# Kernel tuning notes

Hardware: AMD Instinct MI355X
Metric: run time of the kernel (lower is better)

Reference implementation:

```python
import jax, jax.numpy as jnp
import numpy as np

N, D, H = 4_000_000, 10, 16

def setup_inputs() -> dict:
    key = jax.random.key(0)
    k1, k2, k3, k4, k5 = jax.random.split(key, 5)
    x = jax.random.normal(k1, (N, D), dtype=jnp.float32)
    # torch nn.Linear default init: U(-1/sqrt(fan_in), 1/sqrt(fan_in))
    lim1 = 1.0 / np.sqrt(D)
    lim2 = 1.0 / np.sqrt(H)
    W1 = jax.random.uniform(k2, (H, D), dtype=jnp.float32, minval=-lim1, maxval=lim1)
    b1 = jax.random.uniform(k3, (H,), dtype=jnp.float32, minval=-lim1, maxval=lim1)
    W2 = jax.random.uniform(k4, (1, H), dtype=jnp.float32, minval=-lim2, maxval=lim2)
    b2 = jax.random.uniform(k5, (1,), dtype=jnp.float32, minval=-lim2, maxval=lim2)
    return {"x": x, "W1": W1, "b1": b1, "W2": W2, "b2": b2}

def reference(x, W1, b1, W2, b2):
    gram = x.T @ x                      # [10,10] symmetric Gram matrix
    v, w = jnp.linalg.eigh(gram)        # eigenvalues ascending; w: [10,10]
    y = jnp.maximum(w @ W1.T + b1, 0.0) # fc1 + ReLU -> [10,16]
    y = y @ W2.T + b2                   # fc2 -> [10,1]
    return 0.5 * (jax.nn.sigmoid(y) + 1.0)
```

## Files before the change

### kernel.cpp

```cpp
#include <hip/hip_runtime.h>
#include <math.h>


#define BLK2 256
#define GRID2 1024

__global__ void zero_ws_kernel(double* __restrict__ g) {
  int t = threadIdx.x;
  if (t < 55) g[t] = 0.0;
}

__global__ __launch_bounds__(BLK2) void gram_kernel(const float* __restrict__ x,
                                                    double* __restrict__ g,
                                                    int npairs) {
  float acc[55];
#pragma unroll
  for (int k = 0; k < 55; k++) acc[k] = 0.0f;

  int tid = blockIdx.x * BLK2 + threadIdx.x;
  const int stride = GRID2 * BLK2;

  for (int p = tid; p < npairs; p += stride) {
    const float4* base = (const float4*)(x + (size_t)p * 20);
    float4 q0 = base[0], q1 = base[1], q2 = base[2], q3 = base[3], q4 = base[4];
    float v[20] = {q0.x, q0.y, q0.z, q0.w, q1.x, q1.y, q1.z, q1.w,
                   q2.x, q2.y, q2.z, q2.w, q3.x, q3.y, q3.z, q3.w,
                   q4.x, q4.y, q4.z, q4.w};
    int k = 0;
#pragma unroll
    for (int i = 0; i < 10; i++) {
#pragma unroll
      for (int j = 0; j <= i; j++) {
        acc[k] += v[i] * v[j] + v[10 + i] * v[10 + j];
        k++;
      }
    }
  }

  __shared__ double sred[4][55];
  int lane = threadIdx.x & 63;
  int wv = threadIdx.x >> 6;
#pragma unroll
  for (int k = 0; k < 55; k++) {
    double d = (double)acc[k];
#pragma unroll
    for (int off = 32; off > 0; off >>= 1) d += __shfl_down(d, off, 64);
    if (lane == 0) sred[wv][k] = d;
  }
  __syncthreads();
  if (threadIdx.x < 55) {
    double s = sred[0][threadIdx.x] + sred[1][threadIdx.x] +
               sred[2][threadIdx.x] + sred[3][threadIdx.x];
    atomicAdd(&g[threadIdx.x], s);
  }
}


__device__ __forceinline__ float sf_sign(float a, float b) {
  return (b >= 0.0f) ? fabsf(a) : -fabsf(a);
}

__device__ __forceinline__ float slapy2(float x, float y) {
  float xa = fabsf(x), ya = fabsf(y);
  float w = fmaxf(xa, ya), z = fminf(xa, ya);
  if (z == 0.0f) return w;
  float q = z / w;
  return w * sqrtf(1.0f + q * q);
}

__device__ __forceinline__ void slartg(float f, float g, float* c, float* s, float* r) {
  if (g == 0.0f) {
    *c = 1.0f; *s = 0.0f; *r = f;
  } else if (f == 0.0f) {
    *c = 0.0f; *s = sf_sign(1.0f, g); *r = fabsf(g);
  } else {
    float d = sqrtf(f * f + g * g);
    *c = fabsf(f) / d;
    float rr = sf_sign(d, f);
    *s = g / rr;
    *r = rr;
  }
}

__device__ __forceinline__ void slaev2(float a, float b, float c,
                                       float* rt1, float* rt2, float* cs1, float* sn1) {
  float sm = a + c;
  float df = a - c;
  float adf = fabsf(df);
  float tb = b + b;
  float ab = fabsf(tb);
  float acmx, acmn;
  if (fabsf(a) > fabsf(c)) { acmx = a; acmn = c; } else { acmx = c; acmn = a; }
  float rt;
  if (adf > ab)      { float t = ab / adf; rt = adf * sqrtf(1.0f + t * t); }
  else if (adf < ab) { float t = adf / ab; rt = ab * sqrtf(1.0f + t * t); }
  else               { rt = ab * sqrtf(2.0f); }
  int sgn1;
  if (sm < 0.0f) {
    *rt1 = 0.5f * (sm - rt); sgn1 = -1;
    *rt2 = (acmx / *rt1) * acmn - (b / *rt1) * b;
  } else if (sm > 0.0f) {
    *rt1 = 0.5f * (sm + rt); sgn1 = 1;
    *rt2 = (acmx / *rt1) * acmn - (b / *rt1) * b;
  } else {
    *rt1 = 0.5f * rt; *rt2 = -0.5f * rt; sgn1 = 1;
  }
  int sgn2;
  float cs;
  if (df >= 0.0f) { cs = df + rt; sgn2 = 1; } else { cs = df - rt; sgn2 = -1; }
  float acs = fabsf(cs);
  if (acs > ab) {
    float ct = -tb / cs;
    *sn1 = 1.0f / sqrtf(1.0f + ct * ct);
    *cs1 = ct * (*sn1);
  } else {
    if (ab == 0.0f) { *cs1 = 1.0f; *sn1 = 0.0f; }
    else {
      float tn = -cs / tb;
      *cs1 = 1.0f / sqrtf(1.0f + tn * tn);
      *sn1 = tn * (*cs1);
    }
  }
  if (sgn1 == sgn2) { float tn = *cs1; *cs1 = -(*sn1); *sn1 = tn; }
}

__device__ __forceinline__ float sel10(const float* a, int idx0) {
  float v = 0.0f;
#pragma unroll
  for (int k = 0; k < 10; k++) if (k == idx0) v = a[k];
  return v;
}
__device__ __forceinline__ void put10(float* a, int idx0, float v) {
#pragma unroll
  for (int k = 0; k < 10; k++) if (k == idx0) a[k] = v;
}

#define A_(r, c) Am[((r)-1) * 10 + ((c)-1)]
#define Z_(r, c) Zm[((r)-1) * 10 + ((c)-1)]
#define D_(i) dv[(i)-1]
#define E_(i) ev[(i)-1]
#define TAUV(i) tauv[(i)-1]
#define WV(i) wvv[(i)-1]
#define CS_(i) csv[(i)-1]
#define SN_(i) snv[(i)-1]

__global__ __launch_bounds__(64, 1) void eig_mlp_kernel(
    const double* __restrict__ g,
    const float* __restrict__ W1,
    const float* __restrict__ b1,
    const float* __restrict__ W2,
    const float* __restrict__ b2,
    float* __restrict__ out) {
  if (threadIdx.x != 0 || blockIdx.x != 0) return;
  const int n = 10;
  float Am[100], Zm[100];
  float dv[10], ev[10], tauv[10], wvv[10], csv[10], snv[10];

  {
    int k = 0;
#pragma unroll
    for (int i = 0; i < 10; i++)
#pragma unroll
      for (int j = 0; j <= i; j++) {
        float v = (float)g[k++];
        Am[i * 10 + j] = v;
        Am[j * 10 + i] = v;
      }
  }

#pragma unroll
  for (int i = 1; i <= n - 1; i++) {
    const int nmi = n - i;
    float alpha = A_(i + 1, i);
    float taui = 0.0f;
    if (nmi > 1) {
      float ss = 0.0f;
#pragma unroll
      for (int r = i + 2; r <= n; r++) { float t = A_(r, i); ss += t * t; }
      float xnorm = sqrtf(ss);
      if (xnorm != 0.0f) {
        float beta = -sf_sign(slapy2(alpha, xnorm), alpha);
        taui = (beta - alpha) / beta;
        float sc = 1.0f / (alpha - beta);
#pragma unroll
        for (int r = i + 2; r <= n; r++) A_(r, i) *= sc;
        alpha = beta;
      }
    }
    E_(i) = alpha;
    A_(i + 1, i) = alpha;
    if (taui != 0.0f) {
      A_(i + 1, i) = 1.0f;
#pragma unroll
      for (int r = i + 1; r <= n; r++) {
        float s = 0.0f;
#pragma unroll
        for (int c = i + 1; c <= n; c++) {
          float arc = (r >= c) ? A_(r, c) : A_(c, r);
          s += arc * A_(c, i);
        }
        WV(r) = taui * s;
      }
      float dot = 0.0f;
#pragma unroll
      for (int r = i + 1; r <= n; r++) dot += WV(r) * A_(r, i);
      float al2 = -0.5f * taui * dot;
#pragma unroll
      for (int r = i + 1; r <= n; r++) WV(r) += al2 * A_(r, i);
#pragma unroll
      for (int c = i + 1; c <= n; c++)
#pragma unroll
        for (int r = c; r <= n; r++)
          A_(r, c) -= A_(r, i) * WV(c) + WV(r) * A_(c, i);
      A_(i + 1, i) = E_(i);
    }
    D_(i) = A_(i, i);
    TAUV(i) = taui;
  }
  D_(n) = A_(n, n);

#pragma unroll
  for (int r = 1; r <= n; r++)
#pragma unroll
    for (int c = 1; c <= n; c++) Z_(r, c) = (r == c) ? 1.0f : 0.0f;
#pragma unroll
  for (int i = n - 1; i >= 1; i--) {
    float taui = TAUV(i);
    if (taui != 0.0f) {
#pragma unroll
      for (int c = 1; c <= n; c++) {
        float t = Z_(i + 1, c);
#pragma unroll
        for (int r = i + 2; r <= n; r++) t += A_(r, i) * Z_(r, c);
        t *= taui;
        Z_(i + 1, c) -= t;
#pragma unroll
        for (int r = i + 2; r <= n; r++) Z_(r, c) -= A_(r, i) * t;
      }
    }
  }

  const float eps = 5.9604644775390625e-08f;
  const float eps2 = eps * eps;
  const float safmin = 1.17549435082228751e-38f;
  const int nmaxit = n * 30;
  int jtot = 0;
  int l1 = 1;
  int guard = 0;

  while (l1 <= n && guard++ < 2000) {
    int m;
    if (l1 > 1) put10(ev, l1 - 2, 0.0f);
    {
      bool found = false;
      int mf = n;
#pragma unroll
      for (int k = 1; k <= n - 1; k++) {
        if (!found && k >= l1) {
          float tst = fabsf(ev[k - 1]);
          if (tst == 0.0f) {
            mf = k; found = true;
          } else if (tst <= (sqrtf(fabsf(dv[k - 1])) * sqrtf(fabsf(dv[k]))) * eps) {
            ev[k - 1] = 0.0f;
            mf = k; found = true;
          }
        }
      }
      m = found ? mf : n;
    }
    int l = l1, lsv = l, lend = m, lendsv = m;
    l1 = m + 1;
    if (lend == l) continue;
    if (fabsf(sel10(dv, lend - 1)) < fabsf(sel10(dv, l - 1))) { lend = lsv; l = lendsv; }

    if (lend > l) {
      for (;;) {
        if (guard++ > 4000) break;
        int m2;
        if (l != lend) {
          bool found = false;
          int mf = lend;
#pragma unroll
          for (int k = 1; k <= n - 1; k++) {
            if (!found && k >= l && k <= lend - 1) {
              float tst = ev[k - 1] * ev[k - 1];
              if (tst <= (eps2 * fabsf(dv[k - 1])) * fabsf(dv[k]) + safmin) {
                mf = k; found = true;
              }
            }
          }
          m2 = found ? mf : lend;
        } else {
          m2 = lend;
        }
        if (m2 < lend) put10(ev, m2 - 1, 0.0f);
        float p = sel10(dv, l - 1);
        if (m2 == l) {
          put10(dv, l - 1, p);
          l = l + 1;
          if (l <= lend) continue;
          break;
        }
        if (m2 == l + 1) {
          float rt1, rt2, c2, s2;
          slaev2(sel10(dv, l - 1), sel10(ev, l - 1), sel10(dv, l), &rt1, &rt2, &c2, &s2);
#pragma unroll
          for (int j = 1; j <= n - 1; j++) {
            if (j == l) {
#pragma unroll
              for (int r = 0; r < n; r++) {
                float t = Zm[r * 10 + j];
                Zm[r * 10 + j]     = c2 * t - s2 * Zm[r * 10 + j - 1];
                Zm[r * 10 + j - 1] = s2 * t + c2 * Zm[r * 10 + j - 1];
              }
            }
          }
          put10(dv, l - 1, rt1);
          put10(dv, l, rt2);
          put10(ev, l - 1, 0.0f);
          l = l + 2;
          if (l <= lend) continue;
          break;
        }
        if (jtot == nmaxit) break;
        jtot++;
        float El = sel10(ev, l - 1);
        float gg = (sel10(dv, l) - p) / (2.0f * El);
        float rr = slapy2(gg, 1.0f);
        gg = sel10(dv, m2 - 1) - p + (El / (gg + sf_sign(rr, gg)));
        float s = 1.0f, c = 1.0f;
        p = 0.0f;
#pragma unroll
        for (int i = n - 1; i >= 1; i--) {
          if (i <= m2 - 1 && i >= l) {
            float f = s * ev[i - 1];
            float b = c * ev[i - 1];
            slartg(gg, f, &c, &s, &rr);
            if (i != m2 - 1) ev[i] = rr;
            gg = dv[i] - p;
            rr = (dv[i - 1] - gg) * s + 2.0f * c * b;
            p = s * rr;
            dv[i] = gg + p;
            gg = c * rr - b;
            csv[i - 1] = c;
            snv[i - 1] = -s;
          }
        }
#pragma unroll
        for (int j = n - 1; j >= 1; j--) {
          if (j <= m2 - 1 && j >= l) {
            float cj = csv[j - 1], sj = snv[j - 1];
#pragma unroll
            for (int r = 0; r < n; r++) {
              float t = Zm[r * 10 + j];
              Zm[r * 10 + j]     = cj * t - sj * Zm[r * 10 + j - 1];
              Zm[r * 10 + j - 1] = sj * t + cj * Zm[r * 10 + j - 1];
            }
          }
        }
        put10(dv, l - 1, sel10(dv, l - 1) - p);
        put10(ev, l - 1, gg);
      }
    } else {
      for (;;) {
        if (guard++ > 4000) break;
        int m2;
        if (l != lend) {
          bool found = false;
          int mf = lend;
#pragma unroll
          for (int k = n; k >= 2; k--) {
            if (!found && k <= l && k >= lend + 1) {
              float tst = ev[k - 2] * ev[k - 2];
              if (tst <= (eps2 * fabsf(dv[k - 1])) * fabsf(dv[k - 2]) + safmin) {
                mf = k; found = true;
              }
            }
          }
          m2 = found ? mf : lend;
        } else {
          m2 = lend;
        }
        if (m2 > lend) put10(ev, m2 - 2, 0.0f);
        float p = sel10(dv, l - 1);
        if (m2 == l) {
          put10(dv, l - 1, p);
          l = l - 1;
          if (l >= lend) continue;
          break;
        }
        if (m2 == l - 1) {
          float rt1, rt2, c2, s2;
          slaev2(sel10(dv, l - 2), sel10(ev, l - 2), sel10(dv, l - 1), &rt1, &rt2, &c2, &s2);
#pragma unroll
          for (int j = 1; j <= n - 1; j++) {
            if (j == l - 1) {
#pragma unroll
              for (int r = 0; r < n; r++) {
                float t = Zm[r * 10 + j];
                Zm[r * 10 + j]     = c2 * t - s2 * Zm[r * 10 + j - 1];
                Zm[r * 10 + j - 1] = s2 * t + c2 * Zm[r * 10 + j - 1];
              }
            }
          }
          put10(dv, l - 2, rt1);
          put10(dv, l - 1, rt2);
          put10(ev, l - 2, 0.0f);
          l = l - 2;
          if (l >= lend) continue;
          break;
        }
        if (jtot == nmaxit) break;
        jtot++;
        float El1 = sel10(ev, l - 2);
        float gg = (sel10(dv, l - 2) - p) / (2.0f * El1);
        float rr = slapy2(gg, 1.0f);
        gg = sel10(dv, m2 - 1) - p + (El1 / (gg + sf_sign(rr, gg)));
        float s = 1.0f, c = 1.0f;
        p = 0.0f;
#pragma unroll
        for (int i = 1; i <= n - 1; i++) {
          if (i >= m2 && i <= l - 1) {
            float f = s * ev[i - 1];
            float b = c * ev[i - 1];
            slartg(gg, f, &c, &s, &rr);
            if (i >= 2) {
              if (i != m2) ev[i - 2] = rr;
            }
            gg = dv[i - 1] - p;
            rr = (dv[i] - gg) * s + 2.0f * c * b;
            p = s * rr;
            dv[i - 1] = gg + p;
            gg = c * rr - b;
            csv[i - 1] = c;
            snv[i - 1] = s;
          }
        }
#pragma unroll
        for (int j = 1; j <= n - 1; j++) {
          if (j >= m2 && j <= l - 1) {
            float cj = csv[j - 1], sj = snv[j - 1];
#pragma unroll
            for (int r = 0; r < n; r++) {
              float t = Zm[r * 10 + j];
              Zm[r * 10 + j]     = cj * t - sj * Zm[r * 10 + j - 1];
              Zm[r * 10 + j - 1] = sj * t + cj * Zm[r * 10 + j - 1];
            }
          }
        }
        put10(dv, l - 1, sel10(dv, l - 1) - p);
        put10(ev, l - 2, gg);
      }
    }
  }

#pragma unroll
  for (int ii = 2; ii <= n; ii++) {
    const int i = ii - 1;
    int k = i;
    float p = dv[i - 1];
#pragma unroll
    for (int j = ii; j <= n; j++) {
      if (dv[j - 1] < p) { k = j; p = dv[j - 1]; }
    }
    if (k != i) {
      float Di = dv[i - 1];
      put10(dv, k - 1, Di);
      dv[i - 1] = p;
#pragma unroll
      for (int kk = 1; kk <= n; kk++) {
        if (kk == k) {
#pragma unroll
          for (int r = 0; r < n; r++) {
            float t = Zm[r * 10 + (i - 1)];
            Zm[r * 10 + (i - 1)] = Zm[r * 10 + (kk - 1)];
            Zm[r * 10 + (kk - 1)] = t;
          }
        }
      }
    }
  }

#pragma unroll
  for (int r = 0; r < 10; r++) {
    double o = (double)b2[0];
#pragma unroll
    for (int h = 0; h < 16; h++) {
      double sgm = (double)b1[h];
#pragma unroll
      for (int k = 0; k < 10; k++) sgm += (double)Zm[r * 10 + k] * (double)W1[h * 10 + k];
      if (sgm > 0.0) o += sgm * (double)W2[h];
    }
    double sig = 1.0 / (1.0 + exp(-o));
    out[r] = (float)(0.5 * (sig + 1.0));
  }
}

extern "C" void kernel_launch(void* const* d_in, const int* in_sizes, int n_in,
                              void* d_out, int out_size, void* d_ws, size_t ws_size,
                              hipStream_t stream) {
  const float* x  = (const float*)d_in[0];
  const float* W1 = (const float*)d_in[1];
  const float* b1 = (const float*)d_in[2];
  const float* W2 = (const float*)d_in[3];
  const float* b2 = (const float*)d_in[4];
  double* g = (double*)d_ws;
  float* out = (float*)d_out;

  int nrows = in_sizes[0] / 10;
  int npairs = nrows / 2;

  zero_ws_kernel<<<1, 64, 0, stream>>>(g);
  gram_kernel<<<GRID2, BLK2, 0, stream>>>(x, g, npairs);
  eig_mlp_kernel<<<1, 64, 0, stream>>>(g, W1, b1, W2, b2, out);
}
```

Measured before the change: 378.0 us.

## Stage Gram loads through LDS, spread atomics, parallelize eigenvector rotations across lanes

The Gram kernel now reads x as fully coalesced float4 tiles into shared memory and then has each thread pick up its own pair of rows, instead of each thread doing strided 80-byte loads. Block results are spread over four atomic target copies to reduce contention, and the eigensolver kernel summs them. The eigensolver now has each of ten lanes own one row of Z, applying Givens rotations to that row only, with runtime-bounded loops instead of fully unrolled masked loops. This adds two extra barriers per tile and dynamic register indexing via select chains.

```diff
diff --git a/kernel.cpp b/kernel.cpp
--- a/kernel.cpp
+++ b/kernel.cpp
@@ -4,25 +4,52 @@
 
 #define BLK2 256
 #define GRID2 1024
+#define TILE_F4 (BLK2 * 5)
 
 __global__ void zero_ws_kernel(double* __restrict__ g) {
   int t = threadIdx.x;
-  if (t < 55) g[t] = 0.0;
-}
-
-__global__ __launch_bounds__(BLK2) void gram_kernel(const float* __restrict__ x,
+  if (t < 220) g[t] = 0.0;
+}
+
+__global__ __launch_bounds__(BLK2) void gram_kernel(const float4* __restrict__ x4,
                                                     double* __restrict__ g,
-                                                    int npairs) {
+                                                    int nf4) {
+  __shared__ float4 tile[TILE_F4];
   float acc[55];
 #pragma unroll
   for (int k = 0; k < 55; k++) acc[k] = 0.0f;
 
-  int tid = blockIdx.x * BLK2 + threadIdx.x;
-  const int stride = GRID2 * BLK2;
-
-  for (int p = tid; p < npairs; p += stride) {
-    const float4* base = (const float4*)(x + (size_t)p * 20);
-    float4 q0 = base[0], q1 = base[1], q2 = base[2], q3 = base[3], q4 = base[4];
+  const int tid = threadIdx.x;
+  const int ntiles = (nf4 + TILE_F4 - 1) / TILE_F4;
+
+  for (int t = blockIdx.x; t < ntiles; t += GRID2) {
+    const int base = t * TILE_F4;
+    float4 r0, r1, r2, r3, r4;
+    {
+      int i0 = base + 0 * BLK2 + tid;
+      int i1 = base + 1 * BLK2 + tid;
+      int i2 = base + 2 * BLK2 + tid;
+      int i3 = base + 3 * BLK2 + tid;
+      int i4 = base + 4 * BLK2 + tid;
+      float4 zz = make_float4(0.f, 0.f, 0.f, 0.f);
+      r0 = (i0 < nf4) ? x4[i0] : zz;
+      r1 = (i1 < nf4) ? x4[i1] : zz;
+      r2 = (i2 < nf4) ? x4[i2] : zz;
+      r3 = (i3 < nf4) ? x4[i3] : zz;
+      r4 = (i4 < nf4) ? x4[i4] : zz;
+    }
+    __syncthreads();
+    tile[0 * BLK2 + tid] = r0;
+    tile[1 * BLK2 + tid] = r1;
+    tile[2 * BLK2 + tid] = r2;
+    tile[3 * BLK2 + tid] = r3;
+    tile[4 * BLK2 + tid] = r4;
+    __syncthreads();
+    float4 q0 = tile[tid * 5 + 0];
+    float4 q1 = tile[tid * 5 + 1];
+    float4 q2 = tile[tid * 5 + 2];
+    float4 q3 = tile[tid * 5 + 3];
+    float4 q4 = tile[tid * 5 + 4];
     float v[20] = {q0.x, q0.y, q0.z, q0.w, q1.x, q1.y, q1.z, q1.w,
                    q2.x, q2.y, q2.z, q2.w, q3.x, q3.y, q3.z, q3.w,
                    q4.x, q4.y, q4.z, q4.w};
@@ -48,10 +75,11 @@
     if (lane == 0) sred[wv][k] = d;
   }
   __syncthreads();
+  double* gr = g + 55 * (blockIdx.x & 3);
   if (threadIdx.x < 55) {
     double s = sred[0][threadIdx.x] + sred[1][threadIdx.x] +
                sred[2][threadIdx.x] + sred[3][threadIdx.x];
-    atomicAdd(&g[threadIdx.x], s);
+    atomicAdd(&gr[threadIdx.x], s);
   }
 }
 
@@ -127,12 +155,12 @@
 __device__ __forceinline__ float sel10(const float* a, int idx0) {
   float v = 0.0f;
 #pragma unroll
-  for (int k = 0; k < 10; k++) if (k == idx0) v = a[k];
+  for (int k = 0; k < 10; k++) v = (k == idx0) ? a[k] : v;
   return v;
 }
 __device__ __forceinline__ void put10(float* a, int idx0, float v) {
 #pragma unroll
-  for (int k = 0; k < 10; k++) if (k == idx0) a[k] = v;
+  for (int k = 0; k < 10; k++) a[k] = (k == idx0) ? v : a[k];
 }
 
 #define A_(r, c) Am[((r)-1) * 10 + ((c)-1)]
@@ -141,8 +169,6 @@
 #define E_(i) ev[(i)-1]
 #define TAUV(i) tauv[(i)-1]
 #define WV(i) wvv[(i)-1]
-#define CS_(i) csv[(i)-1]
-#define SN_(i) snv[(i)-1]
 
 __global__ __launch_bounds__(64, 1) void eig_mlp_kernel(
     const double* __restrict__ g,
@@ -151,7 +177,8 @@
     const float* __restrict__ W2,
     const float* __restrict__ b2,
     float* __restrict__ out) {
-  if (threadIdx.x != 0 || blockIdx.x != 0) return;
+  if (blockIdx.x != 0) return;
+  const int lane = threadIdx.x;
   const int n = 10;
   float Am[100], Zm[100];
   float dv[10], ev[10], tauv[10], wvv[10], csv[10], snv[10];
@@ -162,9 +189,11 @@
     for (int i = 0; i < 10; i++)
 #pragma unroll
       for (int j = 0; j <= i; j++) {
-        float v = (float)g[k++];
-        Am[i * 10 + j] = v;
-        Am[j * 10 + i] = v;
+        double v = g[k] + g[55 + k] + g[110 + k] + g[165 + k];
+        float f = (float)v;
+        Am[i * 10 + j] = f;
+        Am[j * 10 + i] = f;
+        k++;
       }
   }
 
@@ -238,6 +267,16 @@
         for (int r = i + 2; r <= n; r++) Z_(r, c) -= A_(r, i) * t;
       }
     }
+  }
+
+  const int r_own = (lane < 10) ? lane : 0;
+  float z[10];
+#pragma unroll
+  for (int k = 0; k < 10; k++) {
+    float v = Zm[0 * 10 + k];
+#pragma unroll
+    for (int rr = 1; rr < 10; rr++) v = (r_own == rr) ? Zm[rr * 10 + k] : v;
+    z[k] = v;
   }
 
   const float eps = 5.9604644775390625e-08f;
@@ -249,24 +288,16 @@
   int guard = 0;
 
   while (l1 <= n && guard++ < 2000) {
-    int m;
     if (l1 > 1) put10(ev, l1 - 2, 0.0f);
-    {
-      bool found = false;
-      int mf = n;
-#pragma unroll
-      for (int k = 1; k <= n - 1; k++) {
-        if (!found && k >= l1) {
-          float tst = fabsf(ev[k - 1]);
-          if (tst == 0.0f) {
-            mf = k; found = true;
-          } else if (tst <= (sqrtf(fabsf(dv[k - 1])) * sqrtf(fabsf(dv[k]))) * eps) {
-            ev[k - 1] = 0.0f;
-            mf = k; found = true;
-          }
-        }
-      }
-      m = found ? mf : n;
+    int m = n;
+    for (int mm = l1; mm <= n - 1; mm++) {
+      float tst = fabsf(sel10(ev, mm - 1));
+      if (tst == 0.0f) { m = mm; break; }
+      if (tst <= (sqrtf(fabsf(sel10(dv, mm - 1))) * sqrtf(fabsf(sel10(dv, mm)))) * eps) {
+        put10(ev, mm - 1, 0.0f);
+        m = mm;
+        break;
+      }
     }
     int l = l1, lsv = l, lend = m, lendsv = m;
     l1 = m + 1;
@@ -276,22 +307,15 @@
     if (lend > l) {
       for (;;) {
         if (guard++ > 4000) break;
-        int m2;
+        int m2 = lend;
         if (l != lend) {
-          bool found = false;
-          int mf = lend;
-#pragma unroll
-          for (int k = 1; k <= n - 1; k++) {
-            if (!found && k >= l && k <= lend - 1) {
-              float tst = ev[k - 1] * ev[k - 1];
-              if (tst <= (eps2 * fabsf(dv[k - 1])) * fabsf(dv[k]) + safmin) {
-                mf = k; found = true;
-              }
+          for (int mm = l; mm <= lend - 1; mm++) {
+            float e = sel10(ev, mm - 1);
+            if (e * e <= (eps2 * fabsf(sel10(dv, mm - 1))) * fabsf(sel10(dv, mm)) + safmin) {
+              m2 = mm;
+              break;
             }
           }
-          m2 = found ? mf : lend;
-        } else {
-          m2 = lend;
         }
         if (m2 < lend) put10(ev, m2 - 1, 0.0f);
         float p = sel10(dv, l - 1);
@@ -304,17 +328,10 @@
         if (m2 == l + 1) {
           float rt1, rt2, c2, s2;
           slaev2(sel10(dv, l - 1), sel10(ev, l - 1), sel10(dv, l), &rt1, &rt2, &c2, &s2);
-#pragma unroll
-          for (int j = 1; j <= n - 1; j++) {
-            if (j == l) {
-#pragma unroll
-              for (int r = 0; r < n; r++) {
-                float t = Zm[r * 10 + j];
-                Zm[r * 10 + j]     = c2 * t - s2 * Zm[r * 10 + j - 1];
-                Zm[r * 10 + j - 1] = s2 * t + c2 * Zm[r * 10 + j - 1];
-              }
-            }
-          }
+          float a = sel10(z, l);
+          float b = sel10(z, l - 1);
+          put10(z, l, c2 * a - s2 * b);
+          put10(z, l - 1, s2 * a + c2 * b);
           put10(dv, l - 1, rt1);
           put10(dv, l, rt2);
           put10(ev, l - 1, 0.0f);
@@ -330,33 +347,28 @@
         gg = sel10(dv, m2 - 1) - p + (El / (gg + sf_sign(rr, gg)));
         float s = 1.0f, c = 1.0f;
         p = 0.0f;
-#pragma unroll
-        for (int i = n - 1; i >= 1; i--) {
-          if (i <= m2 - 1 && i >= l) {
-            float f = s * ev[i - 1];
-            float b = c * ev[i - 1];
-            slartg(gg, f, &c, &s, &rr);
-            if (i != m2 - 1) ev[i] = rr;
-            gg = dv[i] - p;
-            rr = (dv[i - 1] - gg) * s + 2.0f * c * b;
-            p = s * rr;
-            dv[i] = gg + p;
-            gg = c * rr - b;
-            csv[i - 1] = c;
-            snv[i - 1] = -s;
+        for (int i = m2 - 1; i >= l; i--) {
+          float e = sel10(ev, i - 1);
+          float f = s * e, b = c * e;
+          slartg(gg, f, &c, &s, &rr);
+          if (i != m2 - 1) put10(ev, i, rr);
+          gg = sel10(dv, i) - p;
+          rr = (sel10(dv, i - 1) - gg) * s + 2.0f * c * b;
+          p = s * rr;
+          put10(dv, i, gg + p);
+          gg = c * rr - b;
+          put10(csv, i - 1, c);
+          put10(snv, i - 1, -s);
+        }
+        {
+          float a = sel10(z, m2 - 1);
+          for (int j = m2 - 1; j >= l; j--) {
+            float cj = sel10(csv, j - 1), sj = sel10(snv, j - 1);
+            float b = sel10(z, j - 1);
+            put10(z, j, cj * a - sj * b);
+            a = sj * a + cj * b;
           }
-        }
-#pragma unroll
-        for (int j = n - 1; j >= 1; j--) {
-          if (j <= m2 - 1 && j >= l) {
-            float cj = csv[j - 1], sj = snv[j - 1];
-#pragma unroll
-            for (int r = 0; r < n; r++) {
-              float t = Zm[r * 10 + j];
-              Zm[r * 10 + j]     = cj * t - sj * Zm[r * 10 + j - 1];
-              Zm[r * 10 + j - 1] = sj * t + cj * Zm[r * 10 + j - 1];
-            }
-          }
+          put10(z, l - 1, a);
         }
         put10(dv, l - 1, sel10(dv, l - 1) - p);
         put10(ev, l - 1, gg);
@@ -364,22 +376,15 @@
     } else {
       for (;;) {
         if (guard++ > 4000) break;
-        int m2;
+        int m2 = lend;
         if (l != lend) {
-          bool found = false;
-          int mf = lend;
-#pragma unroll
-          for (int k = n; k >= 2; k--) {
-            if (!found && k <= l && k >= lend + 1) {
-              float tst = ev[k - 2] * ev[k - 2];
-              if (tst <= (eps2 * fabsf(dv[k - 1])) * fabsf(dv[k - 2]) + safmin) {
-                mf = k; found = true;
-              }
+          for (int mm = l; mm >= lend + 1; mm--) {
+            float e = sel10(ev, mm - 2);
+            if (e * e <= (eps2 * fabsf(sel10(dv, mm - 1))) * fabsf(sel10(dv, mm - 2)) + safmin) {
+              m2 = mm;
+              break;
             }
           }
-          m2 = found ? mf : lend;
-        } else {
-          m2 = lend;
         }
         if (m2 > lend) put10(ev, m2 - 2, 0.0f);
         float p = sel10(dv, l - 1);
@@ -392,17 +397,10 @@
         if (m2 == l - 1) {
           float rt1, rt2, c2, s2;
           slaev2(sel10(dv, l - 2), sel10(ev, l - 2), sel10(dv, l - 1), &rt1, &rt2, &c2, &s2);
-#pragma unroll
-          for (int j = 1; j <= n - 1; j++) {
-            if (j == l - 1) {
-#pragma unroll
-              for (int r = 0; r < n; r++) {
-                float t = Zm[r * 10 + j];
-                Zm[r * 10 + j]     = c2 * t - s2 * Zm[r * 10 + j - 1];
-                Zm[r * 10 + j - 1] = s2 * t + c2 * Zm[r * 10 + j - 1];
-              }
-            }
-          }
+          float a = sel10(z, l - 1);
+          float b = sel10(z, l - 2);
+          put10(z, l - 1, c2 * a - s2 * b);
+          put10(z, l - 2, s2 * a + c2 * b);
           put10(dv, l - 2, rt1);
           put10(dv, l - 1, rt2);
           put10(ev, l - 2, 0.0f);
@@ -418,35 +416,28 @@
         gg = sel10(dv, m2 - 1) - p + (El1 / (gg + sf_sign(rr, gg)));
         float s = 1.0f, c = 1.0f;
         p = 0.0f;
-#pragma unroll
-        for (int i = 1; i <= n - 1; i++) {
-          if (i >= m2 && i <= l - 1) {
-            float f = s * ev[i - 1];
-            float b = c * ev[i - 1];
-            slartg(gg, f, &c, &s, &rr);
-            if (i >= 2) {
-              if (i != m2) ev[i - 2] = rr;
-            }
-            gg = dv[i - 1] - p;
-            rr = (dv[i] - gg) * s + 2.0f * c * b;
-            p = s * rr;
-            dv[i - 1] = gg + p;
-            gg = c * rr - b;
-            csv[i - 1] = c;
-            snv[i - 1] = s;
+        for (int i = m2; i <= l - 1; i++) {
+          float e = sel10(ev, i - 1);
+          float f = s * e, b = c * e;
+          slartg(gg, f, &c, &s, &rr);
+          if (i != m2) put10(ev, i - 2, rr);
+          gg = sel10(dv, i - 1) - p;
+          rr = (sel10(dv, i) - gg) * s + 2.0f * c * b;
+          p = s * rr;
+          put10(dv, i - 1, gg + p);
+          gg = c * rr - b;
+          put10(csv, i - 1, c);
+          put10(snv, i - 1, s);
+        }
+        {
+          float carry = sel10(z, m2 - 1);
+          for (int j = m2; j <= l - 1; j++) {
+            float cj = sel10(csv, j - 1), sj = sel10(snv, j - 1);
+            float t = sel10(z, j);
+            put10(z, j - 1, sj * t + cj * carry);
+            carry = cj * t - sj * carry;
           }
-        }
-#pragma unroll
-        for (int j = 1; j <= n - 1; j++) {
-          if (j >= m2 && j <= l - 1) {
-            float cj = csv[j - 1], sj = snv[j - 1];
-#pragma unroll
-            for (int r = 0; r < n; r++) {
-              float t = Zm[r * 10 + j];
-              Zm[r * 10 + j]     = cj * t - sj * Zm[r * 10 + j - 1];
-              Zm[r * 10 + j - 1] = sj * t + cj * Zm[r * 10 + j - 1];
-            }
-          }
+          put10(z, l - 1, carry);
         }
         put10(dv, l - 1, sel10(dv, l - 1) - p);
         put10(ev, l - 2, gg);
@@ -454,45 +445,35 @@
     }
   }
 
-#pragma unroll
   for (int ii = 2; ii <= n; ii++) {
-    const int i = ii - 1;
+    int i = ii - 1;
     int k = i;
-    float p = dv[i - 1];
-#pragma unroll
+    float p = sel10(dv, i - 1);
     for (int j = ii; j <= n; j++) {
-      if (dv[j - 1] < p) { k = j; p = dv[j - 1]; }
+      float dj = sel10(dv, j - 1);
+      if (dj < p) { k = j; p = dj; }
     }
     if (k != i) {
-      float Di = dv[i - 1];
-      put10(dv, k - 1, Di);
-      dv[i - 1] = p;
-#pragma unroll
-      for (int kk = 1; kk <= n; kk++) {
-        if (kk == k) {
-#pragma unroll
-          for (int r = 0; r < n; r++) {
-            float t = Zm[r * 10 + (i - 1)];
-            Zm[r * 10 + (i - 1)] = Zm[r * 10 + (kk - 1)];
-            Zm[r * 10 + (kk - 1)] = t;
-          }
-        }
-      }
-    }
-  }
-
-#pragma unroll
-  for (int r = 0; r < 10; r++) {
+      float di = sel10(dv, i - 1);
+      put10(dv, k - 1, di);
+      put10(dv, i - 1, p);
+      float a = sel10(z, i - 1), b = sel10(z, k - 1);
+      put10(z, i - 1, b);
+      put10(z, k - 1, a);
+    }
+  }
+
+  if (lane < 10) {
     double o = (double)b2[0];
 #pragma unroll
     for (int h = 0; h < 16; h++) {
       double sgm = (double)b1[h];
 #pragma unroll
-      for (int k = 0; k < 10; k++) sgm += (double)Zm[r * 10 + k] * (double)W1[h * 10 + k];
+      for (int k = 0; k < 10; k++) sgm += (double)z[k] * (double)W1[h * 10 + k];
       if (sgm > 0.0) o += sgm * (double)W2[h];
     }
     double sig = 1.0 / (1.0 + exp(-o));
-    out[r] = (float)(0.5 * (sig + 1.0));
+    out[lane] = (float)(0.5 * (sig + 1.0));
   }
 }
 
@@ -507,10 +488,9 @@
   double* g = (double*)d_ws;
   float* out = (float*)d_out;
 
-  int nrows = in_sizes[0] / 10;
-  int npairs = nrows / 2;
-
-  zero_ws_kernel<<<1, 64, 0, stream>>>(g);
-  gram_kernel<<<GRID2, BLK2, 0, stream>>>(x, g, npairs);
+  int nf4 = in_sizes[0] / 4;
+
+  zero_ws_kernel<<<1, 256, 0, stream>>>(g);
+  gram_kernel<<<GRID2, BLK2, 0, stream>>>((const float4*)x, g, nf4);
   eig_mlp_kernel<<<1, 64, 0, stream>>>(g, W1, b1, W2, b2, out);
 }
```

Result: faster. 367.1 us (-2.9%).
